# Kernel optimization log

Hardware: AMD Instinct MI355X
Metric: run time of the kernel (lower is better)

The kernel has to match this reference:

```python
import jax, jax.numpy as jnp
import numpy as np

B, T, D_IN = 64, 512, 512
D_HID, D_OUT = 1024, 512
NUM_DAYS = 24
EPS = 1e-5


def setup_inputs() -> dict:
    key = jax.random.key(0)
    ks = jax.random.split(key, 8)
    x = jax.random.normal(ks[0], (B, T, D_IN), dtype=jnp.float32)
    day_indices = jax.random.randint(ks[1], (B,), 0, NUM_DAYS)
    s1 = 1.0 / np.sqrt(D_IN)
    s2 = 1.0 / np.sqrt(D_HID)
    W1 = jax.random.uniform(ks[2], (NUM_DAYS, D_IN, D_HID), jnp.float32, -s1, s1)
    b1 = jax.random.uniform(ks[3], (NUM_DAYS, D_HID), jnp.float32, -s1, s1)
    W2 = jax.random.uniform(ks[4], (NUM_DAYS, D_HID, D_OUT), jnp.float32, -s2, s2)
    b2 = jax.random.uniform(ks[5], (NUM_DAYS, D_OUT), jnp.float32, -s2, s2)
    gamma = jnp.ones((NUM_DAYS, D_OUT), jnp.float32)
    beta = jnp.zeros((NUM_DAYS, D_OUT), jnp.float32)
    return {"x": x, "day_indices": day_indices, "W1": W1, "b1": b1,
            "W2": W2, "b2": b2, "gamma": gamma, "beta": beta}


def reference(x, day_indices, W1, b1, W2, b2, gamma, beta):
    # Gather each sample's day-specific adapter params, then one batched pass.
    # Equivalent to the per-day mask/gather/scatter loop in the torch module.
    # Dropout is identity (eval mode).
    W1d = W1[day_indices]                      # [B, D_in, D_hid]
    b1d = b1[day_indices][:, None, :]          # [B, 1, D_hid]
    W2d = W2[day_indices]                      # [B, D_hid, D_out]
    b2d = b2[day_indices][:, None, :]          # [B, 1, D_out]
    h = jax.nn.relu(jnp.einsum('btd,bdh->bth', x, W1d) + b1d)
    y = jnp.einsum('bth,bho->bto', h, W2d) + b2d
    # per-day LayerNorm over last dim
    mean = jnp.mean(y, axis=-1, keepdims=True)
    var = jnp.var(y, axis=-1, keepdims=True)
    y_hat = (y - mean) * jax.lax.rsqrt(var + EPS)
    g = gamma[day_indices][:, None, :]
    bt = beta[day_indices][:, None, :]
    return y_hat * g + bt
```

## Files before the change

kernel.cpp:

```cpp
#include <hip/hip_runtime.h>

#define B_    64
#define T_    512
#define DIN   512
#define DHID  1024
#define DOUT  512
#define NDAYS 24

typedef unsigned short u16;
typedef __bf16 bf16x8 __attribute__((ext_vector_type(8)));
typedef u16    u16x8  __attribute__((ext_vector_type(8)));
typedef float  f32x4  __attribute__((ext_vector_type(4)));

static __device__ __forceinline__ u16 f2bf(float f) {
    union { float f; unsigned u; } v; v.f = f;
    unsigned r = v.u + 0x7FFFu + ((v.u >> 16) & 1u);
    return (u16)(r >> 16);
}
static __device__ __forceinline__ float bf2f(u16 h) {
    union { unsigned u; float f; } v; v.u = ((unsigned)h) << 16;
    return v.f;
}

static __device__ __forceinline__ void gload_lds16(const void* g, void* l) {
    __builtin_amdgcn_global_load_lds(
        (const __attribute__((address_space(1))) void*)g,
        (__attribute__((address_space(3))) void*)l, 16, 0, 0);
}

static __device__ __forceinline__ void transpose64_body(
    const float* __restrict__ W, u16* __restrict__ WT,
    int R, int C, int j, int tid)
{
    __shared__ float t[64][65];
    const int gx = C >> 6, gy = R >> 6;
    const int bx = j % gx;
    const int by = (j / gx) % gy;
    const int d  = j / (gx * gy);
    const int r0 = by * 64, c0 = bx * 64;
    const float* Wd = W + (size_t)d * R * C;
    u16* WTd = WT + (size_t)d * R * C;

#pragma unroll
    for (int i = 0; i < 4; ++i) {
        const int row = i * 16 + (tid >> 4);
        const int col = (tid & 15) * 4;
        const float4 v = *(const float4*)&Wd[(size_t)(r0 + row) * C + c0 + col];
        t[row][col]     = v.x;
        t[row][col + 1] = v.y;
        t[row][col + 2] = v.z;
        t[row][col + 3] = v.w;
    }
    __syncthreads();
#pragma unroll
    for (int p = 0; p < 2; ++p) {
        const int c  = p * 32 + (tid >> 3);
        const int rs = (tid & 7) * 8;
        u16x8 o;
#pragma unroll
        for (int k = 0; k < 8; ++k) o[k] = f2bf(t[rs + k][c]);
        *(u16x8*)&WTd[(size_t)(c0 + c) * R + r0 + rs] = o;
    }
}

__global__ __launch_bounds__(256)
void transpose64(const float* __restrict__ W, u16* __restrict__ WT, int R, int C) {
    transpose64_body(W, WT, R, C, blockIdx.x, threadIdx.x);
}

__global__ __launch_bounds__(256)
void aux_prep(const float* __restrict__ W1, u16* __restrict__ W1T,
              const float* __restrict__ W2, u16* __restrict__ W2T,
              const float* __restrict__ x, u16* __restrict__ xb,
              int nW2)
{
    const int jb = blockIdx.x;
    const int tid = threadIdx.x;
    constexpr int NW1 = NDAYS * (DIN / 64) * (DHID / 64);
    if (jb < NW1) {
        transpose64_body(W1, W1T, DIN, DHID, jb, tid);
    } else if (jb < NW1 + nW2) {
        transpose64_body(W2, W2T, DHID, DOUT, jb - NW1, tid);
    } else {
        const int n8 = B_ * T_ * DIN / 8;
        const int ncvt = gridDim.x - NW1 - nW2;
        int i = (jb - NW1 - nW2) * 256 + tid;
        const int stride = ncvt * 256;
        for (; i < n8; i += stride) {
            float4 a = ((const float4*)x)[i * 2];
            float4 b = ((const float4*)x)[i * 2 + 1];
            u16x8 p;
            p[0] = f2bf(a.x); p[1] = f2bf(a.y); p[2] = f2bf(a.z); p[3] = f2bf(a.w);
            p[4] = f2bf(b.x); p[5] = f2bf(b.y); p[6] = f2bf(b.z); p[7] = f2bf(b.w);
            ((u16x8*)xb)[i] = p;
        }
    }
}

template<int MT, int NT, int KT, bool RELU>
__global__ __launch_bounds__(512, 1)
void gemm8(const u16* __restrict__ Aall,
           const u16* __restrict__ BT,
           const float* __restrict__ bias,
           const int* __restrict__ didx,
           u16* __restrict__ Call)
{
    constexpr int GX = MT / 256;
    constexpr int GY = NT / 256;
    constexpr int NWG = GX * GY * B_;
    constexpr int NT_K = KT / 64;
    static_assert(NT_K >= 2 && (NWG % 8) == 0, "geometry");

    constexpr int Q = NWG / 8;
    const int hw = blockIdx.x;
    const int l  = (hw & 7) * Q + (hw >> 3);
    const int bx = l % GX;
    const int by = (l / GX) % GY;
    const int bz = l / (GX * GY);

    const int day = didx[bz];
    const int m0 = bx * 256, n0 = by * 256;
    const int tid = threadIdx.x;
    const int wv = tid >> 6, ln = tid & 63;
    const int wm = wv >> 2, wn = wv & 3;

    __shared__ __align__(16) u16 smem[4][256 * 64];

    const u16* Ab = Aall + (size_t)bz * MT * KT + (size_t)m0 * KT;
    const u16* Bt = BT + (size_t)day * NT * KT + (size_t)n0 * KT;

    auto stageA = [&](int buf, int t, int h) {
#pragma unroll
        for (int c = 0; c < 2; ++c) {
            const int rl = h * 128 + wv * 16 + c * 8 + (ln >> 3);
            const int cd = (ln & 7) ^ (rl & 7);
            gload_lds16(Ab + (size_t)rl * KT + t * 64 + cd * 8,
                        (char*)&smem[buf][(h * 128 + wv * 16 + c * 8) * 64]);
        }
    };
    auto stageB = [&](int buf, int t, int h) {
#pragma unroll
        for (int c = 0; c < 2; ++c) {
            const int rl = h * 128 + wv * 16 + c * 8 + (ln >> 3);
            const int cd = (ln & 7) ^ (rl & 7);
            gload_lds16(Bt + (size_t)rl * KT + t * 64 + cd * 8,
                        (char*)&smem[2 + buf][(h * 128 + wv * 16 + c * 8) * 64]);
        }
    };

    f32x4 acc[8][4];
#pragma unroll
    for (int i = 0; i < 8; ++i)
#pragma unroll
        for (int j = 0; j < 4; ++j)
            acc[i][j] = (f32x4){0.f, 0.f, 0.f, 0.f};

    stageA(0, 0, 0); stageB(0, 0, 0); stageA(0, 0, 1); stageB(0, 0, 1);
    stageA(1, 1, 0); stageB(1, 1, 0);
    asm volatile("s_waitcnt vmcnt(4)" ::: "memory");
    __builtin_amdgcn_s_barrier();

    for (int t = 0; t < NT_K; ++t) {
        const int buf = t & 1;
        const u16* sAb = smem[buf];
        const u16* sBb = smem[2 + buf];
        bf16x8 av0[2][4], av1[2][4], bv0[2][2], bv1[2][2];

        auto readAv = [&](bf16x8 (&dst)[2][4], int mq) {
#pragma unroll
            for (int ks = 0; ks < 2; ++ks)
#pragma unroll
                for (int mi = 0; mi < 4; ++mi) {
                    const int r = mq * 128 + wm * 64 + mi * 16 + (ln & 15);
                    const int slot = (ks * 4 + (ln >> 4)) ^ (r & 7);
                    dst[ks][mi] = *(const bf16x8*)&sAb[r * 64 + slot * 8];
                }
        };
        auto readBv = [&](bf16x8 (&dst)[2][2], int nq) {
#pragma unroll
            for (int ks = 0; ks < 2; ++ks)
#pragma unroll
                for (int ni = 0; ni < 2; ++ni) {
                    const int r = nq * 128 + wn * 32 + ni * 16 + (ln & 15);
                    const int slot = (ks * 4 + (ln >> 4)) ^ (r & 7);
                    dst[ks][ni] = *(const bf16x8*)&sBb[r * 64 + slot * 8];
                }
        };
        auto mfmaQ = [&](bf16x8 (&a)[2][4], bf16x8 (&b)[2][2], int mq, int nq) {
#pragma unroll
            for (int ks = 0; ks < 2; ++ks)
#pragma unroll
                for (int mi = 0; mi < 4; ++mi)
#pragma unroll
                    for (int ni = 0; ni < 2; ++ni)
                        acc[mq * 4 + mi][nq * 2 + ni] =
                            __builtin_amdgcn_mfma_f32_16x16x32_bf16(
                                a[ks][mi], b[ks][ni],
                                acc[mq * 4 + mi][nq * 2 + ni], 0, 0, 0);
        };

        readAv(av0, 0); readAv(av1, 1); readBv(bv0, 0);
        if (t + 1 < NT_K) { stageA(buf ^ 1, t + 1, 1); stageB(buf ^ 1, t + 1, 1); }
        __builtin_amdgcn_s_barrier();
        asm volatile("s_waitcnt lgkmcnt(0)" ::: "memory");
        __builtin_amdgcn_sched_barrier(0);
        __builtin_amdgcn_s_setprio(1);
        mfmaQ(av0, bv0, 0, 0);
        mfmaQ(av1, bv0, 1, 0);
        __builtin_amdgcn_s_setprio(0);
        __builtin_amdgcn_s_barrier();

        readBv(bv1, 1);
        if (t + 2 < NT_K) { stageA(buf, t + 2, 0); stageB(buf, t + 2, 0); }
        __builtin_amdgcn_s_barrier();
        asm volatile("s_waitcnt lgkmcnt(0)" ::: "memory");
        __builtin_amdgcn_sched_barrier(0);
        __builtin_amdgcn_s_setprio(1);
        mfmaQ(av1, bv1, 1, 1);
        mfmaQ(av0, bv1, 0, 1);
        __builtin_amdgcn_s_setprio(0);
        if (t + 2 < NT_K) asm volatile("s_waitcnt vmcnt(4)" ::: "memory");
        else              asm volatile("s_waitcnt vmcnt(0)" ::: "memory");
        __builtin_amdgcn_s_barrier();
    }

    const float* bs = bias + (size_t)day * NT + n0;
    float bval[2][2];
#pragma unroll
    for (int nq = 0; nq < 2; ++nq)
#pragma unroll
        for (int ni = 0; ni < 2; ++ni)
            bval[nq][ni] = bs[nq * 128 + wn * 32 + ni * 16 + (ln & 15)];

    u16* yb = &smem[0][0];
#pragma unroll
    for (int mq = 0; mq < 2; ++mq)
#pragma unroll
        for (int mi = 0; mi < 4; ++mi)
#pragma unroll
            for (int nq = 0; nq < 2; ++nq)
#pragma unroll
                for (int ni = 0; ni < 2; ++ni) {
                    const int col = nq * 128 + wn * 32 + ni * 16 + (ln & 15);
#pragma unroll
                    for (int i = 0; i < 4; ++i) {
                        const int row = mq * 128 + wm * 64 + mi * 16 + (ln >> 4) * 4 + i;
                        float v = acc[mq * 4 + mi][nq * 2 + ni][i] + bval[nq][ni];
                        if (RELU) v = fmaxf(v, 0.f);
                        yb[row * 256 + col] = f2bf(v);
                    }
                }
    __syncthreads();

    u16* Hb = Call + (size_t)bz * MT * NT + (size_t)m0 * NT + n0;
#pragma unroll
    for (int j = 0; j < 16; ++j) {
        const int row = wv * 32 + j * 2 + (ln >> 5);
        const u16x8 v = *(const u16x8*)&yb[row * 256 + (ln & 31) * 8];
        *(u16x8*)&Hb[(size_t)row * NT + (ln & 31) * 8] = v;
    }
}

__global__ __launch_bounds__(512, 1)
void gemm2_ln(const u16* __restrict__ Aall,
              const u16* __restrict__ BT,
              const float* __restrict__ bias,
              const int* __restrict__ didx,
              const float* __restrict__ gamma,
              const float* __restrict__ beta,
              float* __restrict__ out)
{
    constexpr int BM = 128, BK = 64;
    constexpr int KT = DHID;
    constexpr int NT_K = KT / BK;
    constexpr int GX = T_ / BM;
    constexpr int NWG = GX * B_;

    constexpr int Q = NWG / 8;
    const int hw = blockIdx.x;
    const int l  = (hw & 7) * Q + (hw >> 3);
    const int bx = l % GX;
    const int bz = l / GX;

    const int day = didx[bz];
    const int m0 = bx * BM;
    const int tid = threadIdx.x;
    const int wv = tid >> 6, ln = tid & 63;
    const int wm = wv >> 2, wn = wv & 3;

    __shared__ __align__(16) u16 sA[2][BM * BK];
    __shared__ __align__(16) u16 sB[2][DOUT * BK];

    const u16* Ab = Aall + (size_t)bz * T_ * KT + (size_t)m0 * KT;
    const u16* Bt = BT + (size_t)day * DOUT * KT;

    auto stageA = [&](int buf, int t) {
#pragma unroll
        for (int c = 0; c < 2; ++c) {
            const int rl = wv * 16 + c * 8 + (ln >> 3);
            const int cd = (ln & 7) ^ (rl & 7);
            gload_lds16(Ab + (size_t)rl * KT + t * BK + cd * 8,
                        (char*)&sA[buf][(wv * 16 + c * 8) * BK]);
        }
    };
    auto stageBh = [&](int buf, int t, int h) {
#pragma unroll
        for (int c = 0; c < 4; ++c) {
            const int rl = h * 256 + wv * 32 + c * 8 + (ln >> 3);
            const int cd = (ln & 7) ^ (rl & 7);
            gload_lds16(Bt + (size_t)rl * KT + t * BK + cd * 8,
                        (char*)&sB[buf][(h * 256 + wv * 32 + c * 8) * BK]);
        }
    };

    f32x4 acc[4][8];
#pragma unroll
    for (int i = 0; i < 4; ++i)
#pragma unroll
        for (int j = 0; j < 8; ++j)
            acc[i][j] = (f32x4){0.f, 0.f, 0.f, 0.f};

    stageA(0, 0); stageBh(0, 0, 0); stageBh(0, 0, 1);
    stageA(1, 1); stageBh(1, 1, 0);
    asm volatile("s_waitcnt vmcnt(5)" ::: "memory");
    __builtin_amdgcn_s_barrier();

    for (int t = 0; t < NT_K; ++t) {
        const int buf = t & 1;
        const u16* sAb = sA[buf];
        const u16* sBb = sB[buf];
        bf16x8 av[2][4], bvA[2][2], bvB[2][2];

        auto readBv = [&](bf16x8 (&dst)[2][2], int nq) {
#pragma unroll
            for (int ks = 0; ks < 2; ++ks)
#pragma unroll
                for (int ni = 0; ni < 2; ++ni) {
                    const int r = nq * 128 + wn * 32 + ni * 16 + (ln & 15);
                    const int slot = (ks * 4 + (ln >> 4)) ^ (r & 7);
                    dst[ks][ni] = *(const bf16x8*)&sBb[r * BK + slot * 8];
                }
        };
        auto mfmaQ = [&](bf16x8 (&b)[2][2], int nq) {
#pragma unroll
            for (int ks = 0; ks < 2; ++ks)
#pragma unroll
                for (int mi = 0; mi < 4; ++mi)
#pragma unroll
                    for (int ni = 0; ni < 2; ++ni)
                        acc[mi][nq * 2 + ni] =
                            __builtin_amdgcn_mfma_f32_16x16x32_bf16(
                                av[ks][mi], b[ks][ni],
                                acc[mi][nq * 2 + ni], 0, 0, 0);
        };

#pragma unroll
        for (int ks = 0; ks < 2; ++ks)
#pragma unroll
            for (int mi = 0; mi < 4; ++mi) {
                const int r = wm * 64 + mi * 16 + (ln & 15);
                const int slot = (ks * 4 + (ln >> 4)) ^ (r & 7);
                av[ks][mi] = *(const bf16x8*)&sAb[r * BK + slot * 8];
            }
        readBv(bvA, 0); readBv(bvB, 1);
        if (t + 1 < NT_K) stageBh(buf ^ 1, t + 1, 1);
        __builtin_amdgcn_s_barrier();
        asm volatile("s_waitcnt lgkmcnt(0)" ::: "memory");
        __builtin_amdgcn_sched_barrier(0);
        __builtin_amdgcn_s_setprio(1);
        mfmaQ(bvA, 0);
        mfmaQ(bvB, 1);
        __builtin_amdgcn_s_setprio(0);
        __builtin_amdgcn_s_barrier();

        readBv(bvA, 2); readBv(bvB, 3);
        if (t + 2 < NT_K) { stageA(buf, t + 2); stageBh(buf, t + 2, 0); }
        __builtin_amdgcn_s_barrier();
        asm volatile("s_waitcnt lgkmcnt(0)" ::: "memory");
        __builtin_amdgcn_sched_barrier(0);
        __builtin_amdgcn_s_setprio(1);
        mfmaQ(bvA, 2);
        mfmaQ(bvB, 3);
        __builtin_amdgcn_s_setprio(0);
        if (t + 2 < NT_K) asm volatile("s_waitcnt vmcnt(5)" ::: "memory");
        else              asm volatile("s_waitcnt vmcnt(0)" ::: "memory");
        __builtin_amdgcn_s_barrier();
    }

    const float* bs = bias + (size_t)day * DOUT;
    float bval[8];
#pragma unroll
    for (int f = 0; f < 8; ++f)
        bval[f] = bs[(f >> 1) * 128 + wn * 32 + (f & 1) * 16 + (ln & 15)];

    u16* yb = (u16*)&sB[0][0];
#pragma unroll
    for (int mi = 0; mi < 4; ++mi)
#pragma unroll
        for (int f = 0; f < 8; ++f) {
            const int col = (f >> 1) * 128 + wn * 32 + (f & 1) * 16 + (ln & 15);
#pragma unroll
            for (int i = 0; i < 4; ++i) {
                const int rloc = wm * 64 + mi * 16 + (ln >> 4) * 4 + i;
                yb[rloc * DOUT + col] = f2bf(acc[mi][f][i] + bval[f]);
            }
        }
    __syncthreads();

    const float* gs = gamma + (size_t)day * DOUT;
    const float* es = beta + (size_t)day * DOUT;
    const float4 g0 = ((const float4*)gs)[ln * 2];
    const float4 g1 = ((const float4*)gs)[ln * 2 + 1];
    const float4 e0 = ((const float4*)es)[ln * 2];
    const float4 e1 = ((const float4*)es)[ln * 2 + 1];

    float* op = out + (size_t)bz * T_ * DOUT + (size_t)m0 * DOUT;
#pragma unroll 4
    for (int r = wv * 16; r < wv * 16 + 16; ++r) {
        const u16x8 yv = *(const u16x8*)&yb[r * DOUT + ln * 8];
        float yf[8];
#pragma unroll
        for (int j = 0; j < 8; ++j) yf[j] = bf2f(yv[j]);
        float s = 0.f, q = 0.f;
#pragma unroll
        for (int j = 0; j < 8; ++j) { s += yf[j]; q += yf[j] * yf[j]; }
#pragma unroll
        for (int o = 32; o; o >>= 1) { s += __shfl_xor(s, o); q += __shfl_xor(q, o); }
        const float mean = s * (1.f / 512.f);
        const float var  = q * (1.f / 512.f) - mean * mean;
        const float rstd = rsqrtf(var + 1e-5f);
        float4 o0, o1;
        o0.x = (yf[0] - mean) * rstd * g0.x + e0.x;
        o0.y = (yf[1] - mean) * rstd * g0.y + e0.y;
        o0.z = (yf[2] - mean) * rstd * g0.z + e0.z;
        o0.w = (yf[3] - mean) * rstd * g0.w + e0.w;
        o1.x = (yf[4] - mean) * rstd * g1.x + e1.x;
        o1.y = (yf[5] - mean) * rstd * g1.y + e1.y;
        o1.z = (yf[6] - mean) * rstd * g1.z + e1.z;
        o1.w = (yf[7] - mean) * rstd * g1.w + e1.w;
        ((float4*)(op + (size_t)r * DOUT))[ln * 2] = o0;
        ((float4*)(op + (size_t)r * DOUT))[ln * 2 + 1] = o1;
    }
}

extern "C" void kernel_launch(void* const* d_in, const int* in_sizes, int n_in,
                              void* d_out, int out_size, void* d_ws, size_t ws_size,
                              hipStream_t stream)
{
    const float* x     = (const float*)d_in[0];
    const int*   didx  = (const int*)d_in[1];
    const float* W1    = (const float*)d_in[2];
    const float* b1    = (const float*)d_in[3];
    const float* W2    = (const float*)d_in[4];
    const float* b2    = (const float*)d_in[5];
    const float* gamma = (const float*)d_in[6];
    const float* beta  = (const float*)d_in[7];
    float* out = (float*)d_out;

    char* ws = (char*)d_ws;
    u16* W1T = (u16*)ws;
    u16* h   = (u16*)(ws + 25165824);
    u16* xb  = (u16*)(ws + 92274688);

    const bool bigws = ws_size >= 150994944ULL;
    constexpr int NW = NDAYS * (DIN / 64) * (DHID / 64);

    if (bigws) {
        u16* W2T = (u16*)(ws + 125829120);
        aux_prep<<<NW * 2 + 2048, 256, 0, stream>>>(W1, W1T, W2, W2T, x, xb, NW);
        gemm8<T_, DHID, DIN, true>
            <<<dim3(2 * 4 * B_), 512, 0, stream>>>(xb, W1T, b1, didx, h);
        gemm2_ln<<<dim3(4 * B_), 512, 0, stream>>>(h, W2T, b2, didx, gamma, beta, out);
    } else {
        u16* W2T = xb;
        aux_prep<<<NW + 2048, 256, 0, stream>>>(W1, W1T, W2, W2T, x, xb, 0);
        gemm8<T_, DHID, DIN, true>
            <<<dim3(2 * 4 * B_), 512, 0, stream>>>(xb, W1T, b1, didx, h);
        transpose64<<<NW, 256, 0, stream>>>(W2, W2T, DHID, DOUT);
        gemm2_ln<<<dim3(4 * B_), 512, 0, stream>>>(h, W2T, b2, didx, gamma, beta, out);
    }
}
```

Before: 144.0 us.

## Move W2 transpose into extra blocks of the first GEMM launch

```diff
diff --git a/kernel.cpp b/kernel.cpp
--- a/kernel.cpp
+++ b/kernel.cpp
@@ -28,11 +28,11 @@
         (__attribute__((address_space(3))) void*)l, 16, 0, 0);
 }
 
-static __device__ __forceinline__ void transpose64_body(
+static __device__ __forceinline__ void transpose64_core(
     const float* __restrict__ W, u16* __restrict__ WT,
-    int R, int C, int j, int tid)
+    int R, int C, int j, int tid, float* tbuf)
 {
-    __shared__ float t[64][65];
+    float (*t)[65] = (float(*)[65])tbuf;
     const int gx = C >> 6, gy = R >> 6;
     const int bx = j % gx;
     const int by = (j / gx) % gy;
@@ -65,7 +65,8 @@
 
 __global__ __launch_bounds__(256)
 void transpose64(const float* __restrict__ W, u16* __restrict__ WT, int R, int C) {
-    transpose64_body(W, WT, R, C, blockIdx.x, threadIdx.x);
+    __shared__ float t[64 * 65];
+    transpose64_core(W, WT, R, C, blockIdx.x, threadIdx.x, t);
 }
 
 __global__ __launch_bounds__(256)
@@ -74,13 +75,14 @@
               const float* __restrict__ x, u16* __restrict__ xb,
               int nW2)
 {
+    __shared__ float t[64 * 65];
     const int jb = blockIdx.x;
     const int tid = threadIdx.x;
     constexpr int NW1 = NDAYS * (DIN / 64) * (DHID / 64);
     if (jb < NW1) {
-        transpose64_body(W1, W1T, DIN, DHID, jb, tid);
+        transpose64_core(W1, W1T, DIN, DHID, jb, tid, t);
     } else if (jb < NW1 + nW2) {
-        transpose64_body(W2, W2T, DHID, DOUT, jb - NW1, tid);
+        transpose64_core(W2, W2T, DHID, DOUT, jb - NW1, tid, t);
     } else {
         const int n8 = B_ * T_ * DIN / 8;
         const int ncvt = gridDim.x - NW1 - nW2;
@@ -103,7 +105,9 @@
            const u16* __restrict__ BT,
            const float* __restrict__ bias,
            const int* __restrict__ didx,
-           u16* __restrict__ Call)
+           u16* __restrict__ Call,
+           const float* __restrict__ W2,
+           u16* __restrict__ W2T)
 {
     constexpr int GX = MT / 256;
     constexpr int GY = NT / 256;
@@ -111,8 +115,24 @@
     constexpr int NT_K = KT / 64;
     static_assert(NT_K >= 2 && (NWG % 8) == 0, "geometry");
 
+    __shared__ __align__(16) u16 smem[4][256 * 64];
+
+    const int tid = threadIdx.x;
+    const int hw = blockIdx.x;
+
+    if (hw >= NWG) {
+        float* tb = (float*)&smem[0][0] + (tid >> 8) * (64 * 65);
+        const int t256 = tid & 255;
+        const int base = (hw - NWG) * 4;
+#pragma unroll
+        for (int it = 0; it < 2; ++it) {
+            transpose64_core(W2, W2T, DHID, DOUT, base + it * 2 + (tid >> 8), t256, tb);
+            __syncthreads();
+        }
+        return;
+    }
+
     constexpr int Q = NWG / 8;
-    const int hw = blockIdx.x;
     const int l  = (hw & 7) * Q + (hw >> 3);
     const int bx = l % GX;
     const int by = (l / GX) % GY;
@@ -120,11 +140,8 @@
 
     const int day = didx[bz];
     const int m0 = bx * 256, n0 = by * 256;
-    const int tid = threadIdx.x;
     const int wv = tid >> 6, ln = tid & 63;
     const int wm = wv >> 2, wn = wv & 3;
-
-    __shared__ __align__(16) u16 smem[4][256 * 64];
 
     const u16* Ab = Aall + (size_t)bz * MT * KT + (size_t)m0 * KT;
     const u16* Bt = BT + (size_t)day * NT * KT + (size_t)n0 * KT;
@@ -467,15 +484,15 @@
 
     if (bigws) {
         u16* W2T = (u16*)(ws + 125829120);
-        aux_prep<<<NW * 2 + 2048, 256, 0, stream>>>(W1, W1T, W2, W2T, x, xb, NW);
+        aux_prep<<<NW + 2048, 256, 0, stream>>>(W1, W1T, W2, W2T, x, xb, 0);
         gemm8<T_, DHID, DIN, true>
-            <<<dim3(2 * 4 * B_), 512, 0, stream>>>(xb, W1T, b1, didx, h);
+            <<<dim3(2 * 4 * B_ + NW / 4), 512, 0, stream>>>(xb, W1T, b1, didx, h, W2, W2T);
         gemm2_ln<<<dim3(4 * B_), 512, 0, stream>>>(h, W2T, b2, didx, gamma, beta, out);
     } else {
         u16* W2T = xb;
         aux_prep<<<NW + 2048, 256, 0, stream>>>(W1, W1T, W2, W2T, x, xb, 0);
         gemm8<T_, DHID, DIN, true>
-            <<<dim3(2 * 4 * B_), 512, 0, stream>>>(xb, W1T, b1, didx, h);
+            <<<dim3(2 * 4 * B_), 512, 0, stream>>>(xb, W1T, b1, didx, h, nullptr, nullptr);
         transpose64<<<NW, 256, 0, stream>>>(W2, W2T, DHID, DOUT);
         gemm2_ln<<<dim3(4 * B_), 512, 0, stream>>>(h, W2T, b2, didx, gamma, beta, out);
     }
```

After: 145.7 us. About the same (+1.1%).
